# Kernel optimization log

Hardware: AMD Instinct MI355X
Metric: run time of the kernel (lower is better)

Reference implementation:

```python
import jax, jax.numpy as jnp
import numpy as np

B, L, N_INP, N_HID = 128, 1000, 1, 1024
DT = 0.042
RHO = 0.99
INPUT_SCALING = 1.0
THETA_LIF = 1.0
THETA_RF = 1.0
LIF_TAU_M = 20.0
TAU_REF = 0.25
CONNECTIVITY = 0.1
GAMMA_RANGE = (2.7, 2.9)
EPS_RANGE = (4.7, 4.9)


def setup_inputs() -> dict:
    key = jax.random.key(0)
    x = jax.random.normal(key, (B, L, N_INP), dtype=jnp.float32)
    rng = np.random.default_rng(0)
    # per-unit oscillator params (tuple branch of __init__)
    gamma = rng.uniform(GAMMA_RANGE[0], GAMMA_RANGE[1], N_HID).astype(np.float32)
    epsilon = rng.uniform(EPS_RANGE[0], EPS_RANGE[1], N_HID).astype(np.float32)
    # recurrent matrix: uniform in [-2,2], rescaled to spectral norm rho
    h2h = rng.uniform(-2.0, 2.0, (N_HID, N_HID)).astype(np.float32)
    h2h = h2h * (RHO / np.linalg.norm(h2h, 2)).astype(np.float32)
    x2h = (rng.uniform(0.0, 1.0, (N_INP, N_HID)) * INPUT_SCALING).astype(np.float32)
    bias = ((rng.uniform(0.0, 1.0, N_HID) * 2.0 - 1.0) * INPUT_SCALING).astype(np.float32)
    mask = (rng.uniform(size=(N_HID, N_HID)) < CONNECTIVITY).astype(np.float32)
    lif2hrf = ((rng.uniform(0.0, 1.0, (N_HID, N_HID)) * 2.0 - 1.0) * 2.0 * mask).astype(np.float32)
    return {
        "x": x,
        "x2h": jnp.asarray(x2h),
        "h2h": jnp.asarray(h2h),
        "bias": jnp.asarray(bias),
        "lif2hrf": jnp.asarray(lif2hrf),
        "gamma": jnp.asarray(gamma),
        "epsilon": jnp.asarray(epsilon),
    }


def reference(x, x2h, h2h, bias, lif2hrf, gamma, epsilon):
    dtype = x.dtype
    Bv, Lv, _ = x.shape
    ref_decay = jnp.exp(jnp.asarray(-DT / TAU_REF, dtype))

    def step(carry, xt):
        hy, hz, lif_v, s, ref_p, hy_sum, hy_sq, hrf_n, lif_n = carry
        # input current: (B,I)@(I,H) + (B,H)@(H,H) + (H,)
        cur = xt @ x2h + s @ h2h + bias
        lif_v = lif_v + DT * (-lif_v / LIF_TAU_M + cur)
        lif_s = (lif_v > THETA_LIF).astype(dtype)
        lif_v = lif_v - lif_s * THETA_LIF
        drive = lif_s @ lif2hrf
        hz = hz + DT * (drive - gamma * hy - epsilon * hz)
        hy = hy + DT * hz
        s_new = (hy - THETA_RF - ref_p > 0).astype(dtype)
        # alpha = beta = 0 in bio_cell -> hy, hz unchanged by reset
        ref_p = ref_p * ref_decay + s_new
        hy_sum = hy_sum + hy
        hy_sq = hy_sq + hy * hy
        hrf_n = hrf_n + s_new.sum()
        lif_n = lif_n + lif_s.sum()
        return (hy, hz, lif_v, s_new, ref_p, hy_sum, hy_sq, hrf_n, lif_n), None

    z = jnp.zeros((Bv, N_HID), dtype)
    carry0 = (z, z, z, z, z, z, z, jnp.zeros((), dtype), jnp.zeros((), dtype))
    xs = jnp.swapaxes(x, 0, 1)  # (L, B, I)
    (hy, hz, lif_v, s, ref_p, hy_sum, hy_sq, hrf_n, lif_n), _ = jax.lax.scan(step, carry0, xs)

    hy_mean = hy_sum / Lv
    hy_rms = jnp.sqrt(hy_sq / Lv + 1e-8)
    hy_std = jnp.sqrt(jnp.clip(hy_sq / Lv - hy_mean ** 2, 1e-8))
    features = jnp.concatenate([hy_rms, hy_std, hy], axis=1)  # (B, 3*H)
    denom = Bv * Lv * N_HID
    r_hrf = hrf_n / denom
    r_lif = lif_n / denom
    r_total = r_hrf  # count_lif_spikes=False
    return features, r_total, r_hrf, r_lif
```

## Files before the change

kernel.cpp:

```cpp
#include <hip/hip_runtime.h>

#define NHID    1024
#define BATCH   128
#define LSTEPS  1000
#define DTC     0.042f
#define THETA   1.0f
#define TAUM    20.0f
#define LISTCAP 1032

__global__ __launch_bounds__(1024) void coesn_sim(
    const float* __restrict__ x,
    const float* __restrict__ x2h,
    const float* __restrict__ h2h,
    const float* __restrict__ bias,
    const float* __restrict__ lif2hrf,
    const float* __restrict__ gamma_,
    const float* __restrict__ eps_,
    float* __restrict__ out,
    unsigned int* __restrict__ ws)
{
    const int b    = blockIdx.x;
    const int h    = threadIdx.x;
    const int wv   = h >> 6;
    const int lane = h & 63;
    const int wvs  = __builtin_amdgcn_readfirstlane(wv);

    __shared__ unsigned int Ls[LISTCAP];
    __shared__ unsigned int Ll[LISTCAP];
    __shared__ int Cs[16], Cl[16];
    __shared__ unsigned int red[16];

    Ls[h] = 0; Ll[h] = 0;
    if (h < LISTCAP - 1024) { Ls[1024 + h] = 0; Ll[1024 + h] = 0; }
    if (h < 16) { Cs[h] = 0; Cl[h] = 0; }

    float hy = 0.f, hz = 0.f, v = 0.f, rp = 0.f;
    float hysum = 0.f, hysq = 0.f;
    unsigned int chrf = 0, clif = 0;

    const float g    = gamma_[h];
    const float e    = eps_[h];
    const float bi   = bias[h];
    const float win  = x2h[h];
    const float ref_decay = expf((float)(-0.042 / 0.25));
    const float* xb  = x + (size_t)b * LSTEPS;

    const char* hb = (const char*)h2h     + 4 * (size_t)h;
    const char* lb = (const char*)lif2hrf + 4 * (size_t)h;

    const unsigned long long below = (1ULL << lane) - 1ULL;
    const int l16 = lane & 15;

    int ns = 0;
    float xv_next = xb[0];

    __syncthreads();

    for (int t = 0; t < LSTEPS; ++t) {
        const float xv = xv_next;
        xv_next = xb[(t + 1 < LSTEPS) ? (t + 1) : t];
        float cur = xv * win + bi;
        for (int k = 0; k < ns; k += 8) {
            const unsigned o0 = Ls[k+0], o1 = Ls[k+1], o2 = Ls[k+2], o3 = Ls[k+3];
            const unsigned o4 = Ls[k+4], o5 = Ls[k+5], o6 = Ls[k+6], o7 = Ls[k+7];
            const float a0 = *(const float*)(hb + o0);
            const float a1 = *(const float*)(hb + o1);
            const float a2 = *(const float*)(hb + o2);
            const float a3 = *(const float*)(hb + o3);
            const float a4 = *(const float*)(hb + o4);
            const float a5 = *(const float*)(hb + o5);
            const float a6 = *(const float*)(hb + o6);
            const float a7 = *(const float*)(hb + o7);
            cur += a0;
            cur += (k+1 < ns) ? a1 : 0.0f;
            cur += (k+2 < ns) ? a2 : 0.0f;
            cur += (k+3 < ns) ? a3 : 0.0f;
            cur += (k+4 < ns) ? a4 : 0.0f;
            cur += (k+5 < ns) ? a5 : 0.0f;
            cur += (k+6 < ns) ? a6 : 0.0f;
            cur += (k+7 < ns) ? a7 : 0.0f;
        }

        v = v + DTC * (-v / TAUM + cur);
        const float lsp = (v > THETA) ? 1.f : 0.f;
        v -= lsp * THETA;
        clif += (unsigned)lsp;
        const unsigned long long balL = __ballot(lsp > 0.5f);
        if (lane == 0) Cl[wv] = (int)__popcll(balL);
        __syncthreads();
        int cv = Cl[l16];
        int incl = cv;
        #pragma unroll
        for (int d = 1; d < 16; d <<= 1) {
            const int tt = __shfl_up(incl, d, 16);
            incl += (l16 >= d) ? tt : 0;
        }
        int nl  = __builtin_amdgcn_readlane(incl, 15);
        int pre = __builtin_amdgcn_readlane(incl - cv, wvs);
        if (lsp > 0.5f) Ll[pre + (int)__popcll(balL & below)] = (unsigned)(h * 4096);
        __syncthreads();

        float dr = 0.f;
        for (int k = 0; k < nl; k += 8) {
            const unsigned o0 = Ll[k+0], o1 = Ll[k+1], o2 = Ll[k+2], o3 = Ll[k+3];
            const unsigned o4 = Ll[k+4], o5 = Ll[k+5], o6 = Ll[k+6], o7 = Ll[k+7];
            const float a0 = *(const float*)(lb + o0);
            const float a1 = *(const float*)(lb + o1);
            const float a2 = *(const float*)(lb + o2);
            const float a3 = *(const float*)(lb + o3);
            const float a4 = *(const float*)(lb + o4);
            const float a5 = *(const float*)(lb + o5);
            const float a6 = *(const float*)(lb + o6);
            const float a7 = *(const float*)(lb + o7);
            dr += a0;
            dr += (k+1 < nl) ? a1 : 0.0f;
            dr += (k+2 < nl) ? a2 : 0.0f;
            dr += (k+3 < nl) ? a3 : 0.0f;
            dr += (k+4 < nl) ? a4 : 0.0f;
            dr += (k+5 < nl) ? a5 : 0.0f;
            dr += (k+6 < nl) ? a6 : 0.0f;
            dr += (k+7 < nl) ? a7 : 0.0f;
        }

        hz = hz + DTC * (dr - g * hy - e * hz);
        hy = hy + DTC * hz;
        const float sn = ((hy - THETA - rp) > 0.f) ? 1.f : 0.f;
        rp = rp * ref_decay + sn;
        hysum += hy;
        hysq  += hy * hy;
        chrf += (unsigned)sn;
        const unsigned long long balS = __ballot(sn > 0.5f);
        if (lane == 0) Cs[wv] = (int)__popcll(balS);
        __syncthreads();
        cv = Cs[l16];
        incl = cv;
        #pragma unroll
        for (int d = 1; d < 16; d <<= 1) {
            const int tt = __shfl_up(incl, d, 16);
            incl += (l16 >= d) ? tt : 0;
        }
        ns  = __builtin_amdgcn_readlane(incl, 15);
        pre = __builtin_amdgcn_readlane(incl - cv, wvs);
        if (sn > 0.5f) Ls[pre + (int)__popcll(balS & below)] = (unsigned)(h * 4096);
        __syncthreads();
    }

    const float Lf   = (float)LSTEPS;
    const float mean = hysum / Lf;
    const float rms  = sqrtf(hysq / Lf + 1e-8f);
    float var = hysq / Lf - mean * mean;
    var = fmaxf(var, 1e-8f);
    float* ob = out + (size_t)b * (3 * NHID);
    ob[h]            = rms;
    ob[NHID + h]     = sqrtf(var);
    ob[2 * NHID + h] = hy;

    unsigned int c = chrf;
    for (int off = 32; off > 0; off >>= 1) c += __shfl_down(c, off, 64);
    if (lane == 0) red[wv] = c;
    __syncthreads();
    if (h == 0) {
        unsigned int tot = 0;
        for (int i = 0; i < 16; ++i) tot += red[i];
        ws[b * 2] = tot;
    }
    __syncthreads();
    c = clif;
    for (int off = 32; off > 0; off >>= 1) c += __shfl_down(c, off, 64);
    if (lane == 0) red[wv] = c;
    __syncthreads();
    if (h == 0) {
        unsigned int tot = 0;
        for (int i = 0; i < 16; ++i) tot += red[i];
        ws[b * 2 + 1] = tot;
    }
}

__global__ void coesn_final(const unsigned int* __restrict__ ws,
                            float* __restrict__ out)
{
    if (threadIdx.x == 0 && blockIdx.x == 0) {
        unsigned long long hrf = 0, lif = 0;
        for (int b = 0; b < BATCH; ++b) {
            hrf += ws[b * 2];
            lif += ws[b * 2 + 1];
        }
        const float denom = (float)BATCH * (float)LSTEPS * (float)NHID;
        const float r_hrf = (float)hrf / denom;
        const float r_lif = (float)lif / denom;
        float* s = out + (size_t)BATCH * 3 * NHID;
        s[0] = r_hrf;
        s[1] = r_hrf;
        s[2] = r_lif;
    }
}

extern "C" void kernel_launch(void* const* d_in, const int* in_sizes, int n_in,
                              void* d_out, int out_size, void* d_ws, size_t ws_size,
                              hipStream_t stream) {
    const float* x       = (const float*)d_in[0];
    const float* x2h     = (const float*)d_in[1];
    const float* h2h     = (const float*)d_in[2];
    const float* bias    = (const float*)d_in[3];
    const float* lif2hrf = (const float*)d_in[4];
    const float* gamma_  = (const float*)d_in[5];
    const float* eps_    = (const float*)d_in[6];
    float* out = (float*)d_out;
    unsigned int* wsp = (unsigned int*)d_ws;

    coesn_sim<<<BATCH, NHID, 0, stream>>>(x, x2h, h2h, bias, lif2hrf, gamma_, eps_, out, wsp);
    coesn_final<<<1, 64, 0, stream>>>(wsp, out);
}
```

Measured before the change: 1.512 ms.

## Process two hidden units per thread with float2 gathers in 512-thread blocks

Each thread now owns two adjacent hidden units, so a block is 512 threads (8 waves) instead of 1024 and the spike lists are walked with float2 gathers. The intent is to halve the LDS list reads and global load instructions per spike and to make the per-step barriers and prefix scans cheaper with fewer waves. The cost is more work per thread and less latency hiding, since fewer waves are in flight per CU across the serial time loop. List ordering still follows increasing unit index, so the sums keep the same order.

```diff
diff --git a/kernel.cpp b/kernel.cpp
--- a/kernel.cpp
+++ b/kernel.cpp
@@ -6,9 +6,10 @@
 #define DTC     0.042f
 #define THETA   1.0f
 #define TAUM    20.0f
+#define NT      512
 #define LISTCAP 1032
 
-__global__ __launch_bounds__(1024) void coesn_sim(
+__global__ __launch_bounds__(NT) void coesn_sim(
     const float* __restrict__ x,
     const float* __restrict__ x2h,
     const float* __restrict__ h2h,
@@ -20,36 +21,39 @@
     unsigned int* __restrict__ ws)
 {
     const int b    = blockIdx.x;
-    const int h    = threadIdx.x;
-    const int wv   = h >> 6;
-    const int lane = h & 63;
+    const int tid  = threadIdx.x;
+    const int wv   = tid >> 6;
+    const int lane = tid & 63;
     const int wvs  = __builtin_amdgcn_readfirstlane(wv);
+    const int l8   = lane & 7;
 
     __shared__ unsigned int Ls[LISTCAP];
     __shared__ unsigned int Ll[LISTCAP];
-    __shared__ int Cs[16], Cl[16];
-    __shared__ unsigned int red[16];
-
-    Ls[h] = 0; Ll[h] = 0;
-    if (h < LISTCAP - 1024) { Ls[1024 + h] = 0; Ll[1024 + h] = 0; }
-    if (h < 16) { Cs[h] = 0; Cl[h] = 0; }
-
-    float hy = 0.f, hz = 0.f, v = 0.f, rp = 0.f;
-    float hysum = 0.f, hysq = 0.f;
+    __shared__ int Cs[8], Cl[8];
+    __shared__ unsigned int red[8];
+
+    Ls[tid] = 0; Ls[tid + 512] = 0;
+    Ll[tid] = 0; Ll[tid + 512] = 0;
+    if (tid < LISTCAP - 1024) { Ls[1024 + tid] = 0; Ll[1024 + tid] = 0; }
+    if (tid < 8) { Cs[tid] = 0; Cl[tid] = 0; }
+
+    const int u0 = 2 * tid;
+    const float2 gg = *(const float2*)(gamma_ + u0);
+    const float2 ee = *(const float2*)(eps_  + u0);
+    const float2 bb = *(const float2*)(bias  + u0);
+    const float2 ww = *(const float2*)(x2h   + u0);
+    const float ref_decay = expf((float)(-0.042 / 0.25));
+    const float* xb = x + (size_t)b * LSTEPS;
+
+    const char* hb = (const char*)h2h     + 8 * (size_t)tid;
+    const char* lb = (const char*)lif2hrf + 8 * (size_t)tid;
+
+    float hy0 = 0.f, hy1 = 0.f, hz0 = 0.f, hz1 = 0.f;
+    float v0 = 0.f, v1 = 0.f, rp0 = 0.f, rp1 = 0.f;
+    float hysum0 = 0.f, hysum1 = 0.f, hysq0 = 0.f, hysq1 = 0.f;
     unsigned int chrf = 0, clif = 0;
 
-    const float g    = gamma_[h];
-    const float e    = eps_[h];
-    const float bi   = bias[h];
-    const float win  = x2h[h];
-    const float ref_decay = expf((float)(-0.042 / 0.25));
-    const float* xb  = x + (size_t)b * LSTEPS;
-
-    const char* hb = (const char*)h2h     + 4 * (size_t)h;
-    const char* lb = (const char*)lif2hrf + 4 * (size_t)h;
-
     const unsigned long long below = (1ULL << lane) - 1ULL;
-    const int l16 = lane & 15;
 
     int ns = 0;
     float xv_next = xb[0];
@@ -59,109 +63,135 @@
     for (int t = 0; t < LSTEPS; ++t) {
         const float xv = xv_next;
         xv_next = xb[(t + 1 < LSTEPS) ? (t + 1) : t];
-        float cur = xv * win + bi;
+        float c0 = xv * ww.x + bb.x;
+        float c1 = xv * ww.y + bb.y;
         for (int k = 0; k < ns; k += 8) {
             const unsigned o0 = Ls[k+0], o1 = Ls[k+1], o2 = Ls[k+2], o3 = Ls[k+3];
             const unsigned o4 = Ls[k+4], o5 = Ls[k+5], o6 = Ls[k+6], o7 = Ls[k+7];
-            const float a0 = *(const float*)(hb + o0);
-            const float a1 = *(const float*)(hb + o1);
-            const float a2 = *(const float*)(hb + o2);
-            const float a3 = *(const float*)(hb + o3);
-            const float a4 = *(const float*)(hb + o4);
-            const float a5 = *(const float*)(hb + o5);
-            const float a6 = *(const float*)(hb + o6);
-            const float a7 = *(const float*)(hb + o7);
-            cur += a0;
-            cur += (k+1 < ns) ? a1 : 0.0f;
-            cur += (k+2 < ns) ? a2 : 0.0f;
-            cur += (k+3 < ns) ? a3 : 0.0f;
-            cur += (k+4 < ns) ? a4 : 0.0f;
-            cur += (k+5 < ns) ? a5 : 0.0f;
-            cur += (k+6 < ns) ? a6 : 0.0f;
-            cur += (k+7 < ns) ? a7 : 0.0f;
-        }
-
-        v = v + DTC * (-v / TAUM + cur);
-        const float lsp = (v > THETA) ? 1.f : 0.f;
-        v -= lsp * THETA;
-        clif += (unsigned)lsp;
-        const unsigned long long balL = __ballot(lsp > 0.5f);
-        if (lane == 0) Cl[wv] = (int)__popcll(balL);
-        __syncthreads();
-        int cv = Cl[l16];
+            const float2 a0 = *(const float2*)(hb + o0);
+            const float2 a1 = *(const float2*)(hb + o1);
+            const float2 a2 = *(const float2*)(hb + o2);
+            const float2 a3 = *(const float2*)(hb + o3);
+            const float2 a4 = *(const float2*)(hb + o4);
+            const float2 a5 = *(const float2*)(hb + o5);
+            const float2 a6 = *(const float2*)(hb + o6);
+            const float2 a7 = *(const float2*)(hb + o7);
+            c0 += a0.x;                         c1 += a0.y;
+            c0 += (k+1 < ns) ? a1.x : 0.0f;     c1 += (k+1 < ns) ? a1.y : 0.0f;
+            c0 += (k+2 < ns) ? a2.x : 0.0f;     c1 += (k+2 < ns) ? a2.y : 0.0f;
+            c0 += (k+3 < ns) ? a3.x : 0.0f;     c1 += (k+3 < ns) ? a3.y : 0.0f;
+            c0 += (k+4 < ns) ? a4.x : 0.0f;     c1 += (k+4 < ns) ? a4.y : 0.0f;
+            c0 += (k+5 < ns) ? a5.x : 0.0f;     c1 += (k+5 < ns) ? a5.y : 0.0f;
+            c0 += (k+6 < ns) ? a6.x : 0.0f;     c1 += (k+6 < ns) ? a6.y : 0.0f;
+            c0 += (k+7 < ns) ? a7.x : 0.0f;     c1 += (k+7 < ns) ? a7.y : 0.0f;
+        }
+
+        v0 = v0 + DTC * (-v0 / TAUM + c0);
+        v1 = v1 + DTC * (-v1 / TAUM + c1);
+        const float lsp0 = (v0 > THETA) ? 1.f : 0.f;
+        const float lsp1 = (v1 > THETA) ? 1.f : 0.f;
+        v0 -= lsp0 * THETA;
+        v1 -= lsp1 * THETA;
+        clif += (unsigned)lsp0 + (unsigned)lsp1;
+        const unsigned long long bA = __ballot(lsp0 > 0.5f);
+        const unsigned long long bB = __ballot(lsp1 > 0.5f);
+        if (lane == 0) Cl[wv] = (int)(__popcll(bA) + __popcll(bB));
+        __syncthreads();
+        int cv = Cl[l8];
         int incl = cv;
         #pragma unroll
-        for (int d = 1; d < 16; d <<= 1) {
-            const int tt = __shfl_up(incl, d, 16);
-            incl += (l16 >= d) ? tt : 0;
-        }
-        int nl  = __builtin_amdgcn_readlane(incl, 15);
+        for (int d = 1; d < 8; d <<= 1) {
+            const int tt = __shfl_up(incl, d, 8);
+            incl += (l8 >= d) ? tt : 0;
+        }
+        int nl  = __builtin_amdgcn_readlane(incl, 7);
         int pre = __builtin_amdgcn_readlane(incl - cv, wvs);
-        if (lsp > 0.5f) Ll[pre + (int)__popcll(balL & below)] = (unsigned)(h * 4096);
-        __syncthreads();
-
-        float dr = 0.f;
+        {
+            const int posA = (int)(__popcll(bA & below) + __popcll(bB & below));
+            if (lsp0 > 0.5f) Ll[pre + posA] = (unsigned)(u0 * 4096);
+            if (lsp1 > 0.5f)
+                Ll[pre + posA + (int)((bA >> lane) & 1ULL)] = (unsigned)(u0 * 4096 + 4096);
+        }
+        __syncthreads();
+
+        float d0 = 0.f, d1 = 0.f;
         for (int k = 0; k < nl; k += 8) {
             const unsigned o0 = Ll[k+0], o1 = Ll[k+1], o2 = Ll[k+2], o3 = Ll[k+3];
             const unsigned o4 = Ll[k+4], o5 = Ll[k+5], o6 = Ll[k+6], o7 = Ll[k+7];
-            const float a0 = *(const float*)(lb + o0);
-            const float a1 = *(const float*)(lb + o1);
-            const float a2 = *(const float*)(lb + o2);
-            const float a3 = *(const float*)(lb + o3);
-            const float a4 = *(const float*)(lb + o4);
-            const float a5 = *(const float*)(lb + o5);
-            const float a6 = *(const float*)(lb + o6);
-            const float a7 = *(const float*)(lb + o7);
-            dr += a0;
-            dr += (k+1 < nl) ? a1 : 0.0f;
-            dr += (k+2 < nl) ? a2 : 0.0f;
-            dr += (k+3 < nl) ? a3 : 0.0f;
-            dr += (k+4 < nl) ? a4 : 0.0f;
-            dr += (k+5 < nl) ? a5 : 0.0f;
-            dr += (k+6 < nl) ? a6 : 0.0f;
-            dr += (k+7 < nl) ? a7 : 0.0f;
-        }
-
-        hz = hz + DTC * (dr - g * hy - e * hz);
-        hy = hy + DTC * hz;
-        const float sn = ((hy - THETA - rp) > 0.f) ? 1.f : 0.f;
-        rp = rp * ref_decay + sn;
-        hysum += hy;
-        hysq  += hy * hy;
-        chrf += (unsigned)sn;
-        const unsigned long long balS = __ballot(sn > 0.5f);
-        if (lane == 0) Cs[wv] = (int)__popcll(balS);
-        __syncthreads();
-        cv = Cs[l16];
+            const float2 a0 = *(const float2*)(lb + o0);
+            const float2 a1 = *(const float2*)(lb + o1);
+            const float2 a2 = *(const float2*)(lb + o2);
+            const float2 a3 = *(const float2*)(lb + o3);
+            const float2 a4 = *(const float2*)(lb + o4);
+            const float2 a5 = *(const float2*)(lb + o5);
+            const float2 a6 = *(const float2*)(lb + o6);
+            const float2 a7 = *(const float2*)(lb + o7);
+            d0 += a0.x;                         d1 += a0.y;
+            d0 += (k+1 < nl) ? a1.x : 0.0f;     d1 += (k+1 < nl) ? a1.y : 0.0f;
+            d0 += (k+2 < nl) ? a2.x : 0.0f;     d1 += (k+2 < nl) ? a2.y : 0.0f;
+            d0 += (k+3 < nl) ? a3.x : 0.0f;     d1 += (k+3 < nl) ? a3.y : 0.0f;
+            d0 += (k+4 < nl) ? a4.x : 0.0f;     d1 += (k+4 < nl) ? a4.y : 0.0f;
+            d0 += (k+5 < nl) ? a5.x : 0.0f;     d1 += (k+5 < nl) ? a5.y : 0.0f;
+            d0 += (k+6 < nl) ? a6.x : 0.0f;     d1 += (k+6 < nl) ? a6.y : 0.0f;
+            d0 += (k+7 < nl) ? a7.x : 0.0f;     d1 += (k+7 < nl) ? a7.y : 0.0f;
+        }
+
+        hz0 = hz0 + DTC * (d0 - gg.x * hy0 - ee.x * hz0);
+        hz1 = hz1 + DTC * (d1 - gg.y * hy1 - ee.y * hz1);
+        hy0 = hy0 + DTC * hz0;
+        hy1 = hy1 + DTC * hz1;
+        const float sn0 = ((hy0 - THETA - rp0) > 0.f) ? 1.f : 0.f;
+        const float sn1 = ((hy1 - THETA - rp1) > 0.f) ? 1.f : 0.f;
+        rp0 = rp0 * ref_decay + sn0;
+        rp1 = rp1 * ref_decay + sn1;
+        hysum0 += hy0; hysq0 += hy0 * hy0;
+        hysum1 += hy1; hysq1 += hy1 * hy1;
+        chrf += (unsigned)sn0 + (unsigned)sn1;
+        const unsigned long long sA = __ballot(sn0 > 0.5f);
+        const unsigned long long sB = __ballot(sn1 > 0.5f);
+        if (lane == 0) Cs[wv] = (int)(__popcll(sA) + __popcll(sB));
+        __syncthreads();
+        cv = Cs[l8];
         incl = cv;
         #pragma unroll
-        for (int d = 1; d < 16; d <<= 1) {
-            const int tt = __shfl_up(incl, d, 16);
-            incl += (l16 >= d) ? tt : 0;
-        }
-        ns  = __builtin_amdgcn_readlane(incl, 15);
+        for (int d = 1; d < 8; d <<= 1) {
+            const int tt = __shfl_up(incl, d, 8);
+            incl += (l8 >= d) ? tt : 0;
+        }
+        ns  = __builtin_amdgcn_readlane(incl, 7);
         pre = __builtin_amdgcn_readlane(incl - cv, wvs);
-        if (sn > 0.5f) Ls[pre + (int)__popcll(balS & below)] = (unsigned)(h * 4096);
-        __syncthreads();
-    }
-
-    const float Lf   = (float)LSTEPS;
-    const float mean = hysum / Lf;
-    const float rms  = sqrtf(hysq / Lf + 1e-8f);
-    float var = hysq / Lf - mean * mean;
-    var = fmaxf(var, 1e-8f);
+        {
+            const int posA = (int)(__popcll(sA & below) + __popcll(sB & below));
+            if (sn0 > 0.5f) Ls[pre + posA] = (unsigned)(u0 * 4096);
+            if (sn1 > 0.5f)
+                Ls[pre + posA + (int)((sA >> lane) & 1ULL)] = (unsigned)(u0 * 4096 + 4096);
+        }
+        __syncthreads();
+    }
+
+    const float Lf = (float)LSTEPS;
     float* ob = out + (size_t)b * (3 * NHID);
-    ob[h]            = rms;
-    ob[NHID + h]     = sqrtf(var);
-    ob[2 * NHID + h] = hy;
+    {
+        const float mean0 = hysum0 / Lf;
+        const float mean1 = hysum1 / Lf;
+        const float rms0  = sqrtf(hysq0 / Lf + 1e-8f);
+        const float rms1  = sqrtf(hysq1 / Lf + 1e-8f);
+        float var0 = hysq0 / Lf - mean0 * mean0;
+        float var1 = hysq1 / Lf - mean1 * mean1;
+        var0 = fmaxf(var0, 1e-8f);
+        var1 = fmaxf(var1, 1e-8f);
+        *(float2*)(ob + u0)            = make_float2(rms0, rms1);
+        *(float2*)(ob + NHID + u0)     = make_float2(sqrtf(var0), sqrtf(var1));
+        *(float2*)(ob + 2 * NHID + u0) = make_float2(hy0, hy1);
+    }
 
     unsigned int c = chrf;
     for (int off = 32; off > 0; off >>= 1) c += __shfl_down(c, off, 64);
     if (lane == 0) red[wv] = c;
     __syncthreads();
-    if (h == 0) {
+    if (tid == 0) {
         unsigned int tot = 0;
-        for (int i = 0; i < 16; ++i) tot += red[i];
+        for (int i = 0; i < 8; ++i) tot += red[i];
         ws[b * 2] = tot;
     }
     __syncthreads();
@@ -169,9 +199,9 @@
     for (int off = 32; off > 0; off >>= 1) c += __shfl_down(c, off, 64);
     if (lane == 0) red[wv] = c;
     __syncthreads();
-    if (h == 0) {
+    if (tid == 0) {
         unsigned int tot = 0;
-        for (int i = 0; i < 16; ++i) tot += red[i];
+        for (int i = 0; i < 8; ++i) tot += red[i];
         ws[b * 2 + 1] = tot;
     }
 }
@@ -208,6 +238,6 @@
     float* out = (float*)d_out;
     unsigned int* wsp = (unsigned int*)d_ws;
 
-    coesn_sim<<<BATCH, NHID, 0, stream>>>(x, x2h, h2h, bias, lif2hrf, gamma_, eps_, out, wsp);
+    coesn_sim<<<BATCH, NT, 0, stream>>>(x, x2h, h2h, bias, lif2hrf, gamma_, eps_, out, wsp);
     coesn_final<<<1, 64, 0, stream>>>(wsp, out);
 }
```

Result: slower. 1.724 ms (+14.0%).
